# Kernel optimization log

Measured on AMD Instinct MI355X. Metric: run time of the kernel, lower is better.

Reference implementation:

```python
import jax, jax.numpy as jnp
import numpy as np

K = 3          # kernel_size
DEG_P = 6      # numerator coeffs (order 5)
DEG_Q = 4      # denominator coeffs (powers 1..4)


def setup_inputs() -> dict:
    key = jax.random.key(0)
    k1, k2, k3 = jax.random.split(key, 3)
    B, Cin, Cout, H, W = 4, 16, 16, 64, 64
    x = jax.random.normal(k1, (B, Cin, H, W), dtype=jnp.float32)
    # per (out_channel f, in_channel c, kernel position p) rational coefficients
    A = jax.random.normal(k2, (Cout, Cin, K * K, DEG_P), dtype=jnp.float32) * 0.1
    Bc = jax.random.normal(k3, (Cout, Cin, K * K, DEG_Q), dtype=jnp.float32) * 0.1
    return {"x": x, "A": A, "Bc": Bc}


def reference(x, A, Bc):
    # x: [B, C, H, W]; A: [F, C, K*K, 6]; Bc: [F, C, K*K, 4]
    B, C, H, W = x.shape
    pad = (K - 1) // 2
    xp = jnp.pad(x, ((0, 0), (0, 0), (pad, pad), (pad, pad)))
    # sliding windows, one slice per kernel offset -> [K*K, B, C, H, W]
    wins = jnp.stack([xp[:, :, i:i + H, j:j + W]
                      for i in range(K) for j in range(K)])
    # powers x^0..x^5 -> [K*K, B, C, H, W, 6]
    pw = wins[..., None] ** jnp.arange(DEG_P, dtype=x.dtype)
    P = jnp.einsum('pbchwi,fcpi->fpbchw', pw, A)
    Q = 1.0 + jnp.abs(jnp.einsum('pbchwi,fcpi->fpbchw', pw[..., 1:1 + DEG_Q], Bc))
    # sum over kernel positions (p) and input channels (c) -> [F, B, H, W]
    out = jnp.sum(P / Q, axis=(1, 3))
    return jnp.transpose(out, (1, 0, 2, 3))  # [B, F, H, W]
```

## Files before the change

kernel.cpp:

```cpp
#include <hip/hip_runtime.h>


#define BB   4
#define CIN  16
#define COUT 16
#define HH   64
#define WW   64

__global__ __launch_bounds__(512, 4) void KAConv_kernel(
    const float* __restrict__ x,
    const float* __restrict__ A,
    const float* __restrict__ Bc,
    float* __restrict__ out)
{
    const int blk   = blockIdx.x;
    const int f     = blk & 15;
    const int rtile = (blk >> 4) & 7;
    const int b     = blk >> 7;

    const int tid  = threadIdx.x;
    const int team = __builtin_amdgcn_readfirstlane(tid >> 8);
    const int tp   = tid & 255;
    const int w    = tp & 63;
    const int r0   = (rtile << 3) + ((tp >> 6) << 1);
    const int c0   = team << 3;

    const float* __restrict__ xb = x  + (b * CIN + c0) * (HH * WW);
    const float* __restrict__ Af = A  + (f * CIN + c0) * 54;
    const float* __restrict__ Bf = Bc + (f * CIN + c0) * 36;

    __shared__ float sRed[2 * 256];

    float acc0 = 0.0f, acc1 = 0.0f;

    for (int c = 0; c < 8; ++c) {
        const float* __restrict__ xc = xb + c * (HH * WW);

        float vv[4][3];
        #pragma unroll
        for (int ri = 0; ri < 4; ++ri) {
            const int hh   = r0 - 1 + ri;
            const bool okh = (hh >= 0) & (hh < HH);
            #pragma unroll
            for (int j = 0; j < 3; ++j) {
                const int wj  = w + j - 1;
                const bool ok = okh & (wj >= 0) & (wj < WW);
                vv[ri][j] = ok ? xc[hh * WW + wj] : 0.0f;
            }
        }

        const float* __restrict__ Ac = Af + c * 54;
        const float* __restrict__ Bq = Bf + c * 36;

        #pragma unroll
        for (int p = 0; p < 9; ++p) {
            const int i = p / 3;
            const int j = p % 3;
            const float va = vv[i][j];
            const float vb = vv[i + 1][j];
            const float* __restrict__ a  = Ac + p * 6;
            const float* __restrict__ bq = Bq + p * 4;

            float P0 = a[5], P1 = a[5];
            P0 = fmaf(P0, va, a[4]);  P1 = fmaf(P1, vb, a[4]);
            P0 = fmaf(P0, va, a[3]);  P1 = fmaf(P1, vb, a[3]);
            P0 = fmaf(P0, va, a[2]);  P1 = fmaf(P1, vb, a[2]);
            P0 = fmaf(P0, va, a[1]);  P1 = fmaf(P1, vb, a[1]);
            P0 = fmaf(P0, va, a[0]);  P1 = fmaf(P1, vb, a[0]);

            float q0 = bq[3], q1 = bq[3];
            q0 = fmaf(q0, va, bq[2]); q1 = fmaf(q1, vb, bq[2]);
            q0 = fmaf(q0, va, bq[1]); q1 = fmaf(q1, vb, bq[1]);
            q0 = fmaf(q0, va, bq[0]); q1 = fmaf(q1, vb, bq[0]);
            q0 *= va;                 q1 *= vb;

            const float d0 = 1.0f + fabsf(q0);
            const float d1 = 1.0f + fabsf(q1);
            acc0 = fmaf(P0, __builtin_amdgcn_rcpf(d0), acc0);
            acc1 = fmaf(P1, __builtin_amdgcn_rcpf(d1), acc1);
        }
    }

    if (team == 1) {
        sRed[tp]       = acc0;
        sRed[256 + tp] = acc1;
    }
    __syncthreads();
    if (team == 0) {
        acc0 += sRed[tp];
        acc1 += sRed[256 + tp];
        float* __restrict__ of = out + ((b * COUT + f) * HH) * WW + w;
        of[r0 * WW]       = acc0;
        of[(r0 + 1) * WW] = acc1;
    }
}

extern "C" void kernel_launch(void* const* d_in, const int* in_sizes, int n_in,
                              void* d_out, int out_size, void* d_ws, size_t ws_size,
                              hipStream_t stream) {
    const float* x  = (const float*)d_in[0];
    const float* A  = (const float*)d_in[1];
    const float* Bc = (const float*)d_in[2];
    float* out = (float*)d_out;

    const int grid = BB * (HH / 8) * COUT;
    KAConv_kernel<<<grid, 512, 0, stream>>>(x, A, Bc, out);
}
```

Baseline: 20.05 us.

## Prefetch next channel's inputs and broadcast coefficients via lane reads

Coefficients for each channel are now loaded as one vector value per lane and broadcast with readlane instead of being fetched through scalar loads. The next channel's window values and coefficients are loaded at the top of each iteration, so memory latency overlaps the current channel's arithmetic. The loop is kept rolled to limit code size. In exchange, register pressure rises and readlane instructions add VALU/SALU work per kernel position.

Result: slower. 27.34 us (+36.3%).

```diff
diff --git a/kernel.cpp b/kernel.cpp
--- a/kernel.cpp
+++ b/kernel.cpp
@@ -6,6 +6,26 @@
 #define COUT 16
 #define HH   64
 #define WW   64
+
+static __device__ __forceinline__ float rdl(float v, int k) {
+    return __int_as_float(__builtin_amdgcn_readlane(__float_as_int(v), k));
+}
+
+static __device__ __forceinline__ void loadw(const float* __restrict__ xb, int c,
+                                             int r0, int w, float v[4][3]) {
+    const float* __restrict__ xc = xb + c * (HH * WW);
+    #pragma unroll
+    for (int ri = 0; ri < 4; ++ri) {
+        const int hh   = r0 - 1 + ri;
+        const bool okh = (hh >= 0) & (hh < HH);
+        #pragma unroll
+        for (int j = 0; j < 3; ++j) {
+            const int wj  = w + j - 1;
+            const bool ok = okh & (wj >= 0) & (wj < WW);
+            v[ri][j] = ok ? xc[hh * WW + wj] : 0.0f;
+        }
+    }
+}
 
 __global__ __launch_bounds__(512, 4) void KAConv_kernel(
     const float* __restrict__ x,
@@ -21,6 +41,7 @@
     const int tid  = threadIdx.x;
     const int team = __builtin_amdgcn_readfirstlane(tid >> 8);
     const int tp   = tid & 255;
+    const int lane = tid & 63;
     const int w    = tp & 63;
     const int r0   = (rtile << 3) + ((tp >> 6) << 1);
     const int c0   = team << 3;
@@ -29,28 +50,25 @@
     const float* __restrict__ Af = A  + (f * CIN + c0) * 54;
     const float* __restrict__ Bf = Bc + (f * CIN + c0) * 36;
 
+    const int laneA = lane < 54 ? lane : 53;
+    const int laneB = lane < 36 ? lane : 35;
+
     __shared__ float sRed[2 * 256];
+
+    float cA = Af[laneA];
+    float cB = Bf[laneB];
+    float vv[4][3];
+    loadw(xb, 0, r0, w, vv);
 
     float acc0 = 0.0f, acc1 = 0.0f;
 
+    #pragma unroll 1
     for (int c = 0; c < 8; ++c) {
-        const float* __restrict__ xc = xb + c * (HH * WW);
-
-        float vv[4][3];
-        #pragma unroll
-        for (int ri = 0; ri < 4; ++ri) {
-            const int hh   = r0 - 1 + ri;
-            const bool okh = (hh >= 0) & (hh < HH);
-            #pragma unroll
-            for (int j = 0; j < 3; ++j) {
-                const int wj  = w + j - 1;
-                const bool ok = okh & (wj >= 0) & (wj < WW);
-                vv[ri][j] = ok ? xc[hh * WW + wj] : 0.0f;
-            }
-        }
-
-        const float* __restrict__ Ac = Af + c * 54;
-        const float* __restrict__ Bq = Bf + c * 36;
+        const int cn = (c + 1 < 8) ? c + 1 : 7;
+        float nA = Af[cn * 54 + laneA];
+        float nB = Bf[cn * 36 + laneB];
+        float vn[4][3];
+        loadw(xb, cn, r0, w, vn);
 
         #pragma unroll
         for (int p = 0; p < 9; ++p) {
@@ -58,27 +76,43 @@
             const int j = p % 3;
             const float va = vv[i][j];
             const float vb = vv[i + 1][j];
-            const float* __restrict__ a  = Ac + p * 6;
-            const float* __restrict__ bq = Bq + p * 4;
 
-            float P0 = a[5], P1 = a[5];
-            P0 = fmaf(P0, va, a[4]);  P1 = fmaf(P1, vb, a[4]);
-            P0 = fmaf(P0, va, a[3]);  P1 = fmaf(P1, vb, a[3]);
-            P0 = fmaf(P0, va, a[2]);  P1 = fmaf(P1, vb, a[2]);
-            P0 = fmaf(P0, va, a[1]);  P1 = fmaf(P1, vb, a[1]);
-            P0 = fmaf(P0, va, a[0]);  P1 = fmaf(P1, vb, a[0]);
+            const float a0 = rdl(cA, p * 6 + 0);
+            const float a1 = rdl(cA, p * 6 + 1);
+            const float a2 = rdl(cA, p * 6 + 2);
+            const float a3 = rdl(cA, p * 6 + 3);
+            const float a4 = rdl(cA, p * 6 + 4);
+            const float a5 = rdl(cA, p * 6 + 5);
+            const float b1 = rdl(cB, p * 4 + 0);
+            const float b2 = rdl(cB, p * 4 + 1);
+            const float b3 = rdl(cB, p * 4 + 2);
+            const float b4 = rdl(cB, p * 4 + 3);
 
-            float q0 = bq[3], q1 = bq[3];
-            q0 = fmaf(q0, va, bq[2]); q1 = fmaf(q1, vb, bq[2]);
-            q0 = fmaf(q0, va, bq[1]); q1 = fmaf(q1, vb, bq[1]);
-            q0 = fmaf(q0, va, bq[0]); q1 = fmaf(q1, vb, bq[0]);
-            q0 *= va;                 q1 *= vb;
+            float P0 = a5, P1 = a5;
+            P0 = fmaf(P0, va, a4);  P1 = fmaf(P1, vb, a4);
+            P0 = fmaf(P0, va, a3);  P1 = fmaf(P1, vb, a3);
+            P0 = fmaf(P0, va, a2);  P1 = fmaf(P1, vb, a2);
+            P0 = fmaf(P0, va, a1);  P1 = fmaf(P1, vb, a1);
+            P0 = fmaf(P0, va, a0);  P1 = fmaf(P1, vb, a0);
+
+            float q0 = b4, q1 = b4;
+            q0 = fmaf(q0, va, b3);  q1 = fmaf(q1, vb, b3);
+            q0 = fmaf(q0, va, b2);  q1 = fmaf(q1, vb, b2);
+            q0 = fmaf(q0, va, b1);  q1 = fmaf(q1, vb, b1);
+            q0 *= va;               q1 *= vb;
 
             const float d0 = 1.0f + fabsf(q0);
             const float d1 = 1.0f + fabsf(q1);
             acc0 = fmaf(P0, __builtin_amdgcn_rcpf(d0), acc0);
             acc1 = fmaf(P1, __builtin_amdgcn_rcpf(d1), acc1);
         }
+
+        cA = nA;  cB = nB;
+        #pragma unroll
+        for (int ri = 0; ri < 4; ++ri)
+            #pragma unroll
+            for (int j = 0; j < 3; ++j)
+                vv[ri][j] = vn[ri][j];
     }
 
     if (team == 1) {
```
